# Performance work log

Measured on AMD Instinct MI355X. Metric: run time of the kernel, lower is better.

## Reference

```python
import jax, jax.numpy as jnp
import numpy as np

EPS = 1e-05
HEAD_DIM = 32


def setup_inputs() -> dict:
    key = jax.random.key(0)
    ks = jax.random.split(key, 8)
    b, c, h, w = 8, 512, 64, 64
    s = 1.0 / np.sqrt(c).astype(np.float32)
    return {
        "q": jax.random.normal(ks[0], (b, c, h, w), jnp.float32),
        "k": jax.random.normal(ks[1], (b, c, h, w), jnp.float32),
        "v": jax.random.normal(ks[2], (b, c, h, w), jnp.float32),
        "Wq": jax.random.normal(ks[3], (c, c), jnp.float32) * s,
        "Wk": jax.random.normal(ks[4], (c, c), jnp.float32) * s,
        "Wv": jax.random.normal(ks[5], (c, c), jnp.float32) * s,
        "Wp": jax.random.normal(ks[6], (c, c), jnp.float32) * s,
        "bp": jax.random.normal(ks[7], (c,), jnp.float32) * 0.02,
    }


def reference(q, k, v, Wq, Wk, Wv, Wp, bp):
    b, c, h, w = q.shape
    n = h * w
    hd = HEAD_DIM
    nh = c // hd

    def proj_heads(x, W):
        # NCHW -> (b, n, c) tokens, then Linear (x @ W.T), then split heads
        t = x.reshape(b, c, n).transpose(0, 2, 1)          # (b, n, c)
        y = jnp.einsum('bnc,dc->bnd', t, W)                # torch Linear: x @ W.T
        return y.reshape(b, n, nh, hd)                     # (b, n, h, d)

    # elu feature map: elu(x) + 1
    Q = jax.nn.elu(proj_heads(q, Wq)) + 1.0
    K = jax.nn.elu(proj_heads(k, Wk)) + 1.0
    V = proj_heads(v, Wv)

    # NOTE: faithful to original einsums — KV contracts over HEADS per token,
    # Z uses K summed over the sequence.
    KV = jnp.einsum('bnhd,bnhm->bnmd', K, V)               # (b, n, d_out=m? -> (b,n,hd,hd))
    Z = 1.0 / (jnp.einsum('bnhd,bhd->bnh', Q, K.sum(axis=1)) + EPS)  # (b, n, h)
    out = jnp.einsum('bnhd,bnmd,bnh->bnhm', Q, KV, Z)      # (b, n, h, m)

    out = out.reshape(b, n, c)                             # merge heads
    out = jnp.einsum('bnc,dc->bnd', out, Wp) + bp          # output projection
    return out.transpose(0, 2, 1).reshape(b, c, h, w)
```

## Files before the change

kernel.cpp:

```cpp
#include <hip/hip_runtime.h>
#include <hip/hip_bf16.h>

#define BATCH 8
#define CD 512
#define NT 4096
#define EPSV 1e-5f

using u16x8 = __attribute__((ext_vector_type(8))) unsigned short;
using u16x4 = __attribute__((ext_vector_type(4))) unsigned short;
using bf8   = __attribute__((ext_vector_type(8))) short;
using f32x4 = __attribute__((ext_vector_type(4))) float;

__device__ __forceinline__ float b2f(unsigned short u) {
    union { unsigned int i; float f; } x; x.i = ((unsigned int)u) << 16; return x.f;
}
__device__ __forceinline__ unsigned short f2b(float f) {
    unsigned int x = __float_as_uint(f);
    unsigned int r = (x + 0x7fffu + ((x >> 16) & 1u)) >> 16;
    return (unsigned short)r;
}
__device__ __forceinline__ unsigned int cvtpk(float a, float b) {
    unsigned int r;
    asm("v_cvt_pk_bf16_f32 %0, %1, %2" : "=v"(r) : "v"(a), "v"(b));
    return r;
}
__device__ __forceinline__ void gload_lds16(const void* g, void* l) {
    __builtin_amdgcn_global_load_lds((const __attribute__((address_space(1))) unsigned int*)g,
                                     (__attribute__((address_space(3))) unsigned int*)l, 16, 0, 0);
}
__device__ __forceinline__ int swz8(int r) { return (r ^ (r >> 3)) & 7; }

__global__ __launch_bounds__(256)
void wconv(const float* __restrict__ W0, const float* __restrict__ W1,
           const float* __restrict__ W2, const float* __restrict__ W3,
           unsigned short* __restrict__ Wb) {
    const float* src = (blockIdx.y == 0) ? W0 : (blockIdx.y == 1) ? W1 : (blockIdx.y == 2) ? W2 : W3;
    unsigned short* dst = Wb + (size_t)blockIdx.y * CD * CD;
    const int base = blockIdx.x * 4096 + threadIdx.x * 16;
    u16x8 o0, o1;
    #pragma unroll
    for (int i = 0; i < 4; ++i) {
        float4 v = *reinterpret_cast<const float4*>(src + base + i * 4);
        unsigned short* t = (i < 2) ? (unsigned short*)&o0 : (unsigned short*)&o1;
        t[(i & 1) * 4 + 0] = f2b(v.x); t[(i & 1) * 4 + 1] = f2b(v.y);
        t[(i & 1) * 4 + 2] = f2b(v.z); t[(i & 1) * 4 + 3] = f2b(v.w);
    }
    *(u16x8*)(dst + base)     = o0;
    *(u16x8*)(dst + base + 8) = o1;
}

__global__ __launch_bounds__(256)
void proj_gemm_all(const float* __restrict__ q, const float* __restrict__ k,
                   const float* __restrict__ v, const unsigned short* __restrict__ Wb,
                   unsigned short* __restrict__ Qp, unsigned short* __restrict__ Kp,
                   unsigned short* __restrict__ Vp, float* __restrict__ Kpart) {
    __shared__ __align__(16) unsigned short Xs[64 * 512];
    __shared__ __align__(16) unsigned short Ws[128 * 64];
    const int nper = gridDim.x >> 3;
    const int work = (blockIdx.x & 7) * nper + (blockIdx.x >> 3);
    const int mat  = work / 512;
    const int rem  = work - mat * 512;
    const int b    = rem >> 6;
    const int tile = rem & 63;
    const int n0   = tile * 64;
    const float* Xb = (mat == 0 ? q : mat == 1 ? k : v) + (size_t)b * CD * NT;
    const unsigned short* W = Wb + (size_t)mat * CD * CD;
    unsigned short* Tb = (mat == 0 ? Qp : mat == 1 ? Kp : Vp) + (size_t)b * NT * CD;
    const int act = (mat < 2);

    const int tid = threadIdx.x, lane = tid & 63, wv = tid >> 6;

    #pragma unroll 4
    for (int i = 0; i < 8; ++i) {
        const int s  = i * 256 + tid;
        const int c0 = (s >> 4) * 4;
        const int t0 = (s & 15) * 4;
        const float* p = Xb + (size_t)c0 * NT + n0 + t0;
        float4 r0 = *(const float4*)(p);
        float4 r1 = *(const float4*)(p + NT);
        float4 r2 = *(const float4*)(p + 2 * NT);
        float4 r3 = *(const float4*)(p + 3 * NT);
        float a0[4] = {r0.x, r0.y, r0.z, r0.w};
        float a1[4] = {r1.x, r1.y, r1.z, r1.w};
        float a2[4] = {r2.x, r2.y, r2.z, r2.w};
        float a3[4] = {r3.x, r3.y, r3.z, r3.w};
        #pragma unroll
        for (int j = 0; j < 4; ++j) {
            uint2 u;
            u.x = cvtpk(a0[j], a1[j]);
            u.y = cvtpk(a2[j], a3[j]);
            const int row  = t0 + j;
            const int byte = (row * 1024 + c0 * 2) ^ (swz8(row) << 4);
            *(uint2*)((char*)Xs + byte) = u;
        }
    }
    __syncthreads();

    for (int d0i = 0; d0i < 4; ++d0i) {
        f32x4 acc[4][2];
        #pragma unroll
        for (int m = 0; m < 4; ++m)
            #pragma unroll
            for (int j = 0; j < 2; ++j)
                acc[m][j] = (f32x4){0.f, 0.f, 0.f, 0.f};

        for (int kc = 0; kc < 8; ++kc) {
            #pragma unroll
            for (int it = 0; it < 4; ++it) {
                const int idx = it * 256 + tid;
                const int r = idx >> 3, p = idx & 7;
                gload_lds16(W + (size_t)(d0i * 128 + r) * CD + kc * 64 + (p ^ swz8(r)) * 8,
                            (char*)Ws + idx * 16);
            }
            __syncthreads();
            #pragma unroll
            for (int kk = 0; kk < 2; ++kk) {
                const int kp = kk * 4 + (lane >> 4);
                bf8 af[4], bfr[2];
                #pragma unroll
                for (int m = 0; m < 4; ++m) {
                    const int r = m * 16 + (lane & 15);
                    af[m] = *(const bf8*)((const char*)Xs +
                            ((r * 1024 + kc * 128 + kp * 16) ^ (swz8(r) << 4)));
                }
                #pragma unroll
                for (int j = 0; j < 2; ++j) {
                    const int rw = wv * 32 + j * 16 + (lane & 15);
                    bfr[j] = *(const bf8*)((const char*)Ws + rw * 128 + ((kp ^ swz8(rw)) * 16));
                }
                #pragma unroll
                for (int m = 0; m < 4; ++m)
                    #pragma unroll
                    for (int j = 0; j < 2; ++j)
                        acc[m][j] = __builtin_amdgcn_mfma_f32_16x16x32_bf16(af[m], bfr[j], acc[m][j], 0, 0, 0);
            }
            __syncthreads();
        }

        float kacc[2] = {0.f, 0.f};
        #pragma unroll
        for (int m = 0; m < 4; ++m) {
            const int ib = n0 + m * 16 + ((lane >> 4) << 2);
            #pragma unroll
            for (int j = 0; j < 2; ++j) {
                const int jb = d0i * 128 + wv * 32 + j * 16 + (lane & 15);
                f32x4 vv = acc[m][j];
                #pragma unroll
                for (int r = 0; r < 4; ++r) {
                    float val = vv[r];
                    if (act) val = (val > 0.f) ? (val + 1.f) : __expf(val);
                    if (mat == 1) kacc[j] += val;
                    Tb[(size_t)(ib + r) * CD + jb] = f2b(val);
                }
            }
        }
        if (mat == 1) {
            #pragma unroll
            for (int j = 0; j < 2; ++j) {
                float s = kacc[j];
                s += __shfl_xor(s, 16, 64);
                s += __shfl_xor(s, 32, 64);
                if (lane < 16) {
                    const int jb = d0i * 128 + wv * 32 + j * 16 + lane;
                    Kpart[(size_t)(b * 64 + tile) * CD + jb] = s;
                }
            }
        }
    }
}

__global__ __launch_bounds__(512)
void ksum_red2(const float* __restrict__ Kpart, float* __restrict__ Ks) {
    const int b = blockIdx.x, c = threadIdx.x;
    float s = 0.f;
    #pragma unroll 8
    for (int t = 0; t < 64; ++t) s += Kpart[(size_t)(b * 64 + t) * CD + c];
    Ks[b * CD + c] = s;
}

__global__ __launch_bounds__(256)
void gemm_final(const unsigned short* __restrict__ Wp, const unsigned short* __restrict__ Tm,
                float* __restrict__ out, const float* __restrict__ bias) {
    __shared__ __align__(16) unsigned short Asm[128 * 64];
    __shared__ __align__(16) unsigned short Bsm[128 * 64];
    const int nper = gridDim.x >> 3;
    const int work = (blockIdx.x & 7) * nper + (blockIdx.x >> 3);
    const int i0 = (work & 3) * 128;
    const int j0 = ((work >> 2) & 31) * 128;
    const int b  = work >> 7;
    const unsigned short* Bb = Tm + (size_t)b * NT * CD;
    const int tid  = threadIdx.x;
    const int lane = tid & 63;
    const int wv   = tid >> 6;
    const int wi = wv >> 1, wj = wv & 1;

    f32x4 acc[4][4];
    #pragma unroll
    for (int m = 0; m < 4; ++m)
        #pragma unroll
        for (int j = 0; j < 4; ++j)
            acc[m][j] = (f32x4){0.f, 0.f, 0.f, 0.f};

    for (int k0 = 0; k0 < CD; k0 += 64) {
        #pragma unroll
        for (int it = 0; it < 4; ++it) {
            const int idx = it * 256 + tid;
            const int r = idx >> 3, p = idx & 7;
            const int ps = p ^ (r & 7);
            gload_lds16(Wp + (size_t)(i0 + r) * CD + k0 + ps * 8, (char*)Asm + idx * 16);
            gload_lds16(Bb + (size_t)(j0 + r) * CD + k0 + ps * 8, (char*)Bsm + idx * 16);
        }
        __syncthreads();
        #pragma unroll
        for (int kk = 0; kk < 2; ++kk) {
            bf8 af[4], bfr[4];
            #pragma unroll
            for (int m = 0; m < 4; ++m) {
                const int r  = wi * 64 + m * 16 + (lane & 15);
                const int kp = kk * 4 + (lane >> 4);
                af[m] = *(const bf8*)((const char*)Asm + r * 128 + ((kp ^ (r & 7)) * 16));
            }
            #pragma unroll
            for (int j = 0; j < 4; ++j) {
                const int r  = wj * 64 + j * 16 + (lane & 15);
                const int kp = kk * 4 + (lane >> 4);
                bfr[j] = *(const bf8*)((const char*)Bsm + r * 128 + ((kp ^ (r & 7)) * 16));
            }
            #pragma unroll
            for (int m = 0; m < 4; ++m)
                #pragma unroll
                for (int j = 0; j < 4; ++j)
                    acc[m][j] = __builtin_amdgcn_mfma_f32_16x16x32_bf16(af[m], bfr[j], acc[m][j], 0, 0, 0);
        }
        __syncthreads();
    }

    #pragma unroll
    for (int m = 0; m < 4; ++m) {
        const int ib = i0 + wi * 64 + m * 16 + (lane >> 4) * 4;
        #pragma unroll
        for (int j = 0; j < 4; ++j) {
            const int jb = j0 + wj * 64 + j * 16 + (lane & 15);
            f32x4 v = acc[m][j];
            #pragma unroll
            for (int r = 0; r < 4; ++r)
                out[(size_t)b * CD * NT + (size_t)(ib + r) * NT + jb] = v[r] + bias[ib + r];
        }
    }
}

__global__ __launch_bounds__(256)
void middle2(const unsigned short* __restrict__ Q, const unsigned short* __restrict__ K,
             const unsigned short* __restrict__ V, const float* __restrict__ Ksum,
             unsigned short* __restrict__ T) {
    __shared__ __align__(16) unsigned short sV[4][512];
    __shared__ __align__(16) unsigned short sP[4][16][32];
    const int b = blockIdx.y;
    const int tid = threadIdx.x;
    const int w = tid >> 6, lane = tid & 63;
    const int r16 = lane & 15, g = lane >> 4;
    const int n0 = blockIdx.x * 16 + w * 4;
    const unsigned short* Qb = Q + ((size_t)b * NT + n0) * CD;
    const unsigned short* Kb = K + ((size_t)b * NT + n0) * CD;
    const unsigned short* Vb = V + ((size_t)b * NT + n0) * CD;
    unsigned short* Tb = T + ((size_t)b * NT + n0) * CD;
    const int fragoff = r16 * 32 + g * 8;

    {
        const int r = lane >> 2, cq = lane & 3;
        *(u16x4*)&sP[w][r][16 + cq * 4] = (u16x4){0, 0, 0, 0};
    }

    const float* ksp = Ksum + b * CD + fragoff;
    float ks[8];
    {
        float4 a0 = *(const float4*)ksp;
        float4 a1 = *(const float4*)(ksp + 4);
        ks[0] = a0.x; ks[1] = a0.y; ks[2] = a0.z; ks[3] = a0.w;
        ks[4] = a1.x; ks[5] = a1.y; ks[6] = a1.z; ks[7] = a1.w;
    }
    unsigned short* sVw = &sV[w][0];

    for (int t = 0; t < 4; ++t) {
        asm volatile("s_waitcnt lgkmcnt(0)" ::: "memory");
        __builtin_amdgcn_sched_barrier(0);
        gload_lds16(Vb + (size_t)t * CD + lane * 8, (char*)sVw + lane * 16);

        const bf8 qf = *(const bf8*)(Qb + (size_t)t * CD + fragoff);
        const bf8 kf = *(const bf8*)(Kb + (size_t)t * CD + fragoff);

        f32x4 s = {0.f, 0.f, 0.f, 0.f};
        s = __builtin_amdgcn_mfma_f32_16x16x32_bf16(kf, qf, s, 0, 0, 0);

        float part = 0.f;
        #pragma unroll
        for (int e = 0; e < 8; ++e) part += b2f((unsigned short)qf[e]) * ks[e];
        part += __shfl_xor(part, 16, 64);
        part += __shfl_xor(part, 32, 64);
        const float z = 1.f / (part + EPSV);

        u16x4 pw;
        #pragma unroll
        for (int r = 0; r < 4; ++r) pw[r] = f2b(s[r] * z);
        *(u16x4*)&sP[w][r16][g * 4] = pw;

        asm volatile("s_waitcnt vmcnt(0) lgkmcnt(0)" ::: "memory");
        __builtin_amdgcn_sched_barrier(0);

        const bf8 pb = *(const bf8*)&sP[w][r16][g * 8];
        bf8 va0 = {}, va1 = {};
        if (g < 2) {
            #pragma unroll
            for (int e = 0; e < 8; ++e) {
                va0[e] = (short)sVw[(g * 8 + e) * 32 + r16];
                va1[e] = (short)sVw[(g * 8 + e) * 32 + 16 + r16];
            }
        }

        f32x4 o0 = {0.f, 0.f, 0.f, 0.f}, o1 = {0.f, 0.f, 0.f, 0.f};
        o0 = __builtin_amdgcn_mfma_f32_16x16x32_bf16(va0, pb, o0, 0, 0, 0);
        o1 = __builtin_amdgcn_mfma_f32_16x16x32_bf16(va1, pb, o1, 0, 0, 0);

        u16x4 w0, w1;
        #pragma unroll
        for (int r = 0; r < 4; ++r) { w0[r] = f2b(o0[r]); w1[r] = f2b(o1[r]); }
        *(u16x4*)(Tb + (size_t)t * CD + r16 * 32 + g * 4)      = w0;
        *(u16x4*)(Tb + (size_t)t * CD + r16 * 32 + 16 + g * 4) = w1;
    }
}

extern "C" void kernel_launch(void* const* d_in, const int* in_sizes, int n_in,
                              void* d_out, int out_size, void* d_ws, size_t ws_size,
                              hipStream_t stream) {
    const float* q  = (const float*)d_in[0];
    const float* k  = (const float*)d_in[1];
    const float* v  = (const float*)d_in[2];
    const float* Wq = (const float*)d_in[3];
    const float* Wk = (const float*)d_in[4];
    const float* Wv = (const float*)d_in[5];
    const float* Wp = (const float*)d_in[6];
    const float* bp = (const float*)d_in[7];
    float* out = (float*)d_out;

    const size_t slab = (size_t)BATCH * NT * CD;
    unsigned short* Qp = (unsigned short*)d_ws;
    unsigned short* Kp = Qp + slab;
    unsigned short* Vp = Kp + slab;
    unsigned short* Tm = Vp + slab;
    unsigned short* Wb = Tm + slab;
    float* Kpart = (float*)(Wb + 4 * (size_t)CD * CD);
    float* Ks    = Kpart + (size_t)512 * CD;

    wconv<<<dim3(64, 4), 256, 0, stream>>>(Wq, Wk, Wv, Wp, Wb);

    const unsigned short* Wpb = Wb + (size_t)3 * CD * CD;

    proj_gemm_all<<<1536, 256, 0, stream>>>(q, k, v, Wb, Qp, Kp, Vp, Kpart);

    ksum_red2<<<8, 512, 0, stream>>>(Kpart, Ks);

    middle2<<<dim3(256, 8), 256, 0, stream>>>(Qp, Kp, Vp, Ks, Tm);

    gemm_final<<<1024, 256, 0, stream>>>(Wpb, Tm, out, bp);
}
```

Baseline: 193.7 us.

## Retile projection GEMM to 128x128 output tiles with streamed fp32 activations

The projection kernel now gives each block a 128-token by 128-channel output tile and streams both W and the fp32 activations through LDS in 64-wide K chunks using async global-to-LDS loads. Before, a block staged a full 64x512 bf16 activation slab once and looped over four output-channel chunks. Activations are converted to bf16 at fragment-load time from fp32 LDS. The output stores are also vectorised along channels in 4-element packs. The aim is better MFMA-to-load ratio and more parallel blocks, at the cost of rereading the activations four times (once per d0 tile) and doing unswizzled fp32 LDS reads that may conflict.

```diff
diff --git a/kernel.cpp b/kernel.cpp
--- a/kernel.cpp
+++ b/kernel.cpp
@@ -28,7 +28,6 @@
     __builtin_amdgcn_global_load_lds((const __attribute__((address_space(1))) unsigned int*)g,
                                      (__attribute__((address_space(3))) unsigned int*)l, 16, 0, 0);
 }
-__device__ __forceinline__ int swz8(int r) { return (r ^ (r >> 3)) & 7; }
 
 __global__ __launch_bounds__(256)
 void wconv(const float* __restrict__ W0, const float* __restrict__ W1,
@@ -54,118 +53,116 @@
                    const float* __restrict__ v, const unsigned short* __restrict__ Wb,
                    unsigned short* __restrict__ Qp, unsigned short* __restrict__ Kp,
                    unsigned short* __restrict__ Vp, float* __restrict__ Kpart) {
-    __shared__ __align__(16) unsigned short Xs[64 * 512];
-    __shared__ __align__(16) unsigned short Ws[128 * 64];
+    __shared__ __align__(16) float          Xf[64 * 128];
+    __shared__ __align__(16) unsigned short Wsm[128 * 64];
     const int nper = gridDim.x >> 3;
     const int work = (blockIdx.x & 7) * nper + (blockIdx.x >> 3);
-    const int mat  = work / 512;
-    const int rem  = work - mat * 512;
-    const int b    = rem >> 6;
-    const int tile = rem & 63;
-    const int n0   = tile * 64;
+    const int mat  = work / 1024;
+    const int rem  = work - mat * 1024;
+    const int b    = rem >> 7;
+    const int rem2 = rem & 127;
+    const int nt   = rem2 >> 2;
+    const int d0   = (rem2 & 3) * 128;
+    const int n0   = nt * 128;
     const float* Xb = (mat == 0 ? q : mat == 1 ? k : v) + (size_t)b * CD * NT;
     const unsigned short* W = Wb + (size_t)mat * CD * CD;
     unsigned short* Tb = (mat == 0 ? Qp : mat == 1 ? Kp : Vp) + (size_t)b * NT * CD;
     const int act = (mat < 2);
 
     const int tid = threadIdx.x, lane = tid & 63, wv = tid >> 6;
-
-    #pragma unroll 4
-    for (int i = 0; i < 8; ++i) {
-        const int s  = i * 256 + tid;
-        const int c0 = (s >> 4) * 4;
-        const int t0 = (s & 15) * 4;
-        const float* p = Xb + (size_t)c0 * NT + n0 + t0;
-        float4 r0 = *(const float4*)(p);
-        float4 r1 = *(const float4*)(p + NT);
-        float4 r2 = *(const float4*)(p + 2 * NT);
-        float4 r3 = *(const float4*)(p + 3 * NT);
-        float a0[4] = {r0.x, r0.y, r0.z, r0.w};
-        float a1[4] = {r1.x, r1.y, r1.z, r1.w};
-        float a2[4] = {r2.x, r2.y, r2.z, r2.w};
-        float a3[4] = {r3.x, r3.y, r3.z, r3.w};
+    const int r16 = lane & 15, g = lane >> 4;
+    const int wi = wv >> 1, wj = wv & 1;
+
+    f32x4 acc[4][4];
+    #pragma unroll
+    for (int m = 0; m < 4; ++m)
+        #pragma unroll
+        for (int j = 0; j < 4; ++j)
+            acc[m][j] = (f32x4){0.f, 0.f, 0.f, 0.f};
+
+    for (int k0 = 0; k0 < CD; k0 += 64) {
+        #pragma unroll
+        for (int it = 0; it < 4; ++it) {
+            const int idx = it * 256 + tid;
+            const int r = idx >> 3, p = idx & 7;
+            const int ps = p ^ (r & 7);
+            gload_lds16(W + (size_t)(d0 + r) * CD + k0 + ps * 8, (char*)Wsm + idx * 16);
+        }
+        #pragma unroll
+        for (int it = 0; it < 8; ++it) {
+            const int idx = it * 256 + tid;
+            const int r = idx >> 5, p = idx & 31;
+            gload_lds16(Xb + (size_t)(k0 + r) * NT + n0 + p * 4, (char*)Xf + idx * 16);
+        }
+        __syncthreads();
+        #pragma unroll
+        for (int kk = 0; kk < 2; ++kk) {
+            const int kp = kk * 4 + g;
+            bf8 af[4], bfr[4];
+            #pragma unroll
+            for (int m = 0; m < 4; ++m) {
+                const int r = wi * 64 + m * 16 + r16;
+                af[m] = *(const bf8*)((const char*)Wsm + r * 128 + ((kp ^ (r & 7)) * 16));
+            }
+            #pragma unroll
+            for (int j = 0; j < 4; ++j) {
+                const int n = wj * 64 + j * 16 + r16;
+                const float* xp = Xf + (kk * 32 + g * 8) * 128 + n;
+                union { uint4 u; bf8 h; } cvt;
+                cvt.u.x = cvtpk(xp[0],   xp[128]);
+                cvt.u.y = cvtpk(xp[256], xp[384]);
+                cvt.u.z = cvtpk(xp[512], xp[640]);
+                cvt.u.w = cvtpk(xp[768], xp[896]);
+                bfr[j] = cvt.h;
+            }
+            #pragma unroll
+            for (int m = 0; m < 4; ++m)
+                #pragma unroll
+                for (int j = 0; j < 4; ++j)
+                    acc[m][j] = __builtin_amdgcn_mfma_f32_16x16x32_bf16(af[m], bfr[j], acc[m][j], 0, 0, 0);
+        }
+        __syncthreads();
+    }
+
+    float kacc[4][4];
+    #pragma unroll
+    for (int m = 0; m < 4; ++m)
+        #pragma unroll
+        for (int r = 0; r < 4; ++r)
+            kacc[m][r] = 0.f;
+
+    #pragma unroll
+    for (int m = 0; m < 4; ++m) {
+        const int db = d0 + wi * 64 + m * 16 + g * 4;
         #pragma unroll
         for (int j = 0; j < 4; ++j) {
-            uint2 u;
-            u.x = cvtpk(a0[j], a1[j]);
-            u.y = cvtpk(a2[j], a3[j]);
-            const int row  = t0 + j;
-            const int byte = (row * 1024 + c0 * 2) ^ (swz8(row) << 4);
-            *(uint2*)((char*)Xs + byte) = u;
-        }
-    }
-    __syncthreads();
-
-    for (int d0i = 0; d0i < 4; ++d0i) {
-        f32x4 acc[4][2];
+            const int n = n0 + wj * 64 + j * 16 + r16;
+            f32x4 vv = acc[m][j];
+            u16x4 pk;
+            #pragma unroll
+            for (int r = 0; r < 4; ++r) {
+                float val = vv[r];
+                if (act) val = (val > 0.f) ? (val + 1.f) : __expf(val);
+                if (mat == 1) kacc[m][r] += val;
+                pk[r] = f2b(val);
+            }
+            *(u16x4*)(Tb + (size_t)n * CD + db) = pk;
+        }
+    }
+    if (mat == 1) {
         #pragma unroll
         for (int m = 0; m < 4; ++m)
             #pragma unroll
-            for (int j = 0; j < 2; ++j)
-                acc[m][j] = (f32x4){0.f, 0.f, 0.f, 0.f};
-
-        for (int kc = 0; kc < 8; ++kc) {
-            #pragma unroll
-            for (int it = 0; it < 4; ++it) {
-                const int idx = it * 256 + tid;
-                const int r = idx >> 3, p = idx & 7;
-                gload_lds16(W + (size_t)(d0i * 128 + r) * CD + kc * 64 + (p ^ swz8(r)) * 8,
-                            (char*)Ws + idx * 16);
-            }
-            __syncthreads();
-            #pragma unroll
-            for (int kk = 0; kk < 2; ++kk) {
-                const int kp = kk * 4 + (lane >> 4);
-                bf8 af[4], bfr[2];
-                #pragma unroll
-                for (int m = 0; m < 4; ++m) {
-                    const int r = m * 16 + (lane & 15);
-                    af[m] = *(const bf8*)((const char*)Xs +
-                            ((r * 1024 + kc * 128 + kp * 16) ^ (swz8(r) << 4)));
+            for (int r = 0; r < 4; ++r) {
+                float s = kacc[m][r];
+                s += __shfl_xor(s, 1, 64);
+                s += __shfl_xor(s, 2, 64);
+                s += __shfl_xor(s, 4, 64);
+                s += __shfl_xor(s, 8, 64);
+                if (r16 == 0) {
+                    Kpart[(size_t)(b * 64 + nt * 2 + wj) * CD + d0 + wi * 64 + m * 16 + g * 4 + r] = s;
                 }
-                #pragma unroll
-                for (int j = 0; j < 2; ++j) {
-                    const int rw = wv * 32 + j * 16 + (lane & 15);
-                    bfr[j] = *(const bf8*)((const char*)Ws + rw * 128 + ((kp ^ swz8(rw)) * 16));
-                }
-                #pragma unroll
-                for (int m = 0; m < 4; ++m)
-                    #pragma unroll
-                    for (int j = 0; j < 2; ++j)
-                        acc[m][j] = __builtin_amdgcn_mfma_f32_16x16x32_bf16(af[m], bfr[j], acc[m][j], 0, 0, 0);
-            }
-            __syncthreads();
-        }
-
-        float kacc[2] = {0.f, 0.f};
-        #pragma unroll
-        for (int m = 0; m < 4; ++m) {
-            const int ib = n0 + m * 16 + ((lane >> 4) << 2);
-            #pragma unroll
-            for (int j = 0; j < 2; ++j) {
-                const int jb = d0i * 128 + wv * 32 + j * 16 + (lane & 15);
-                f32x4 vv = acc[m][j];
-                #pragma unroll
-                for (int r = 0; r < 4; ++r) {
-                    float val = vv[r];
-                    if (act) val = (val > 0.f) ? (val + 1.f) : __expf(val);
-                    if (mat == 1) kacc[j] += val;
-                    Tb[(size_t)(ib + r) * CD + jb] = f2b(val);
-                }
-            }
-        }
-        if (mat == 1) {
-            #pragma unroll
-            for (int j = 0; j < 2; ++j) {
-                float s = kacc[j];
-                s += __shfl_xor(s, 16, 64);
-                s += __shfl_xor(s, 32, 64);
-                if (lane < 16) {
-                    const int jb = d0i * 128 + wv * 32 + j * 16 + lane;
-                    Kpart[(size_t)(b * 64 + tile) * CD + jb] = s;
-                }
-            }
-        }
+            }
     }
 }
 
@@ -355,7 +352,7 @@
 
     const unsigned short* Wpb = Wb + (size_t)3 * CD * CD;
 
-    proj_gemm_all<<<1536, 256, 0, stream>>>(q, k, v, Wb, Qp, Kp, Vp, Kpart);
+    proj_gemm_all<<<3072, 256, 0, stream>>>(q, k, v, Wb, Qp, Kp, Vp, Kpart);
 
     ksum_red2<<<8, 512, 0, stream>>>(Kpart, Ks);
 
```

Result: slower. 219.4 us (+13.3%).

## Retile projection GEMM to 256-token by 64-output blocks with K-chunked X staging

Applied to the files above, without the earlier changes.

Each projection block now computes a 256-token by 64-output tile, streaming both X and W through LDS in 64-wide K chunks instead of holding the whole 64x512 X tile resident. This cuts LDS use per block to raise occupancy and lets loads overlap across more resident blocks. In exchange, the fp32 input activations are re-read and re-converted once per output tile (8 times). The grid doubles and the K-sum partials are written per wave.

```diff
diff --git a/kernel.cpp b/kernel.cpp
--- a/kernel.cpp
+++ b/kernel.cpp
@@ -54,116 +54,114 @@
                    const float* __restrict__ v, const unsigned short* __restrict__ Wb,
                    unsigned short* __restrict__ Qp, unsigned short* __restrict__ Kp,
                    unsigned short* __restrict__ Vp, float* __restrict__ Kpart) {
-    __shared__ __align__(16) unsigned short Xs[64 * 512];
-    __shared__ __align__(16) unsigned short Ws[128 * 64];
+    __shared__ __align__(16) unsigned short Xs[256 * 64];
+    __shared__ __align__(16) unsigned short Ws[64 * 64];
     const int nper = gridDim.x >> 3;
     const int work = (blockIdx.x & 7) * nper + (blockIdx.x >> 3);
-    const int mat  = work / 512;
-    const int rem  = work - mat * 512;
-    const int b    = rem >> 6;
-    const int tile = rem & 63;
-    const int n0   = tile * 64;
+    const int mat  = work / 1024;
+    const int rem  = work - mat * 1024;
+    const int b    = rem >> 7;
+    const int rem2 = rem & 127;
+    const int nt   = rem2 >> 3;
+    const int dt   = rem2 & 7;
+    const int n0   = nt * 256;
+    const int d0   = dt * 64;
     const float* Xb = (mat == 0 ? q : mat == 1 ? k : v) + (size_t)b * CD * NT;
     const unsigned short* W = Wb + (size_t)mat * CD * CD;
     unsigned short* Tb = (mat == 0 ? Qp : mat == 1 ? Kp : Vp) + (size_t)b * NT * CD;
     const int act = (mat < 2);
 
     const int tid = threadIdx.x, lane = tid & 63, wv = tid >> 6;
-
-    #pragma unroll 4
-    for (int i = 0; i < 8; ++i) {
-        const int s  = i * 256 + tid;
-        const int c0 = (s >> 4) * 4;
-        const int t0 = (s & 15) * 4;
-        const float* p = Xb + (size_t)c0 * NT + n0 + t0;
-        float4 r0 = *(const float4*)(p);
-        float4 r1 = *(const float4*)(p + NT);
-        float4 r2 = *(const float4*)(p + 2 * NT);
-        float4 r3 = *(const float4*)(p + 3 * NT);
-        float a0[4] = {r0.x, r0.y, r0.z, r0.w};
-        float a1[4] = {r1.x, r1.y, r1.z, r1.w};
-        float a2[4] = {r2.x, r2.y, r2.z, r2.w};
-        float a3[4] = {r3.x, r3.y, r3.z, r3.w};
+    const int r16 = lane & 15, g = lane >> 4;
+
+    f32x4 acc[4][4];
+    #pragma unroll
+    for (int m = 0; m < 4; ++m)
+        #pragma unroll
+        for (int j = 0; j < 4; ++j)
+            acc[m][j] = (f32x4){0.f, 0.f, 0.f, 0.f};
+
+    for (int kc = 0; kc < 8; ++kc) {
+        #pragma unroll
+        for (int it = 0; it < 2; ++it) {
+            const int idx = it * 256 + tid;
+            const int r = idx >> 3, p = idx & 7;
+            gload_lds16(W + (size_t)(d0 + r) * CD + kc * 64 + (p ^ swz8(r)) * 8,
+                        (char*)Ws + idx * 16);
+        }
+        #pragma unroll
+        for (int i = 0; i < 4; ++i) {
+            const int s  = i * 256 + tid;
+            const int cq = s >> 6;
+            const int nq = s & 63;
+            const float* p = Xb + (size_t)(kc * 64 + cq * 4) * NT + n0 + nq * 4;
+            float4 r0 = *(const float4*)(p);
+            float4 r1 = *(const float4*)(p + NT);
+            float4 r2 = *(const float4*)(p + 2 * NT);
+            float4 r3 = *(const float4*)(p + 3 * NT);
+            float a0[4] = {r0.x, r0.y, r0.z, r0.w};
+            float a1[4] = {r1.x, r1.y, r1.z, r1.w};
+            float a2[4] = {r2.x, r2.y, r2.z, r2.w};
+            float a3[4] = {r3.x, r3.y, r3.z, r3.w};
+            #pragma unroll
+            for (int j = 0; j < 4; ++j) {
+                uint2 u;
+                u.x = cvtpk(a0[j], a1[j]);
+                u.y = cvtpk(a2[j], a3[j]);
+                const int row  = nq * 4 + j;
+                const int byte = (row * 128 + cq * 8) ^ (swz8(row) << 4);
+                *(uint2*)((char*)Xs + byte) = u;
+            }
+        }
+        __syncthreads();
+        #pragma unroll
+        for (int kk = 0; kk < 2; ++kk) {
+            const int kp = kk * 4 + g;
+            bf8 af[4], bfr[4];
+            #pragma unroll
+            for (int m = 0; m < 4; ++m) {
+                const int r = wv * 64 + m * 16 + r16;
+                af[m] = *(const bf8*)((const char*)Xs + ((r * 128 + kp * 16) ^ (swz8(r) << 4)));
+            }
+            #pragma unroll
+            for (int j = 0; j < 4; ++j) {
+                const int rw = j * 16 + r16;
+                bfr[j] = *(const bf8*)((const char*)Ws + rw * 128 + ((kp ^ swz8(rw)) * 16));
+            }
+            #pragma unroll
+            for (int m = 0; m < 4; ++m)
+                #pragma unroll
+                for (int j = 0; j < 4; ++j)
+                    acc[m][j] = __builtin_amdgcn_mfma_f32_16x16x32_bf16(af[m], bfr[j], acc[m][j], 0, 0, 0);
+        }
+        __syncthreads();
+    }
+
+    float kacc[4] = {0.f, 0.f, 0.f, 0.f};
+    #pragma unroll
+    for (int m = 0; m < 4; ++m) {
+        const int ib = n0 + wv * 64 + m * 16 + g * 4;
         #pragma unroll
         for (int j = 0; j < 4; ++j) {
-            uint2 u;
-            u.x = cvtpk(a0[j], a1[j]);
-            u.y = cvtpk(a2[j], a3[j]);
-            const int row  = t0 + j;
-            const int byte = (row * 1024 + c0 * 2) ^ (swz8(row) << 4);
-            *(uint2*)((char*)Xs + byte) = u;
-        }
-    }
-    __syncthreads();
-
-    for (int d0i = 0; d0i < 4; ++d0i) {
-        f32x4 acc[4][2];
-        #pragma unroll
-        for (int m = 0; m < 4; ++m)
-            #pragma unroll
-            for (int j = 0; j < 2; ++j)
-                acc[m][j] = (f32x4){0.f, 0.f, 0.f, 0.f};
-
-        for (int kc = 0; kc < 8; ++kc) {
-            #pragma unroll
-            for (int it = 0; it < 4; ++it) {
-                const int idx = it * 256 + tid;
-                const int r = idx >> 3, p = idx & 7;
-                gload_lds16(W + (size_t)(d0i * 128 + r) * CD + kc * 64 + (p ^ swz8(r)) * 8,
-                            (char*)Ws + idx * 16);
-            }
-            __syncthreads();
-            #pragma unroll
-            for (int kk = 0; kk < 2; ++kk) {
-                const int kp = kk * 4 + (lane >> 4);
-                bf8 af[4], bfr[2];
-                #pragma unroll
-                for (int m = 0; m < 4; ++m) {
-                    const int r = m * 16 + (lane & 15);
-                    af[m] = *(const bf8*)((const char*)Xs +
-                            ((r * 1024 + kc * 128 + kp * 16) ^ (swz8(r) << 4)));
-                }
-                #pragma unroll
-                for (int j = 0; j < 2; ++j) {
-                    const int rw = wv * 32 + j * 16 + (lane & 15);
-                    bfr[j] = *(const bf8*)((const char*)Ws + rw * 128 + ((kp ^ swz8(rw)) * 16));
-                }
-                #pragma unroll
-                for (int m = 0; m < 4; ++m)
-                    #pragma unroll
-                    for (int j = 0; j < 2; ++j)
-                        acc[m][j] = __builtin_amdgcn_mfma_f32_16x16x32_bf16(af[m], bfr[j], acc[m][j], 0, 0, 0);
-            }
-            __syncthreads();
-        }
-
-        float kacc[2] = {0.f, 0.f};
-        #pragma unroll
-        for (int m = 0; m < 4; ++m) {
-            const int ib = n0 + m * 16 + ((lane >> 4) << 2);
-            #pragma unroll
-            for (int j = 0; j < 2; ++j) {
-                const int jb = d0i * 128 + wv * 32 + j * 16 + (lane & 15);
-                f32x4 vv = acc[m][j];
-                #pragma unroll
-                for (int r = 0; r < 4; ++r) {
-                    float val = vv[r];
-                    if (act) val = (val > 0.f) ? (val + 1.f) : __expf(val);
-                    if (mat == 1) kacc[j] += val;
-                    Tb[(size_t)(ib + r) * CD + jb] = f2b(val);
-                }
-            }
-        }
-        if (mat == 1) {
-            #pragma unroll
-            for (int j = 0; j < 2; ++j) {
-                float s = kacc[j];
-                s += __shfl_xor(s, 16, 64);
-                s += __shfl_xor(s, 32, 64);
-                if (lane < 16) {
-                    const int jb = d0i * 128 + wv * 32 + j * 16 + lane;
-                    Kpart[(size_t)(b * 64 + tile) * CD + jb] = s;
-                }
+            const int jb = d0 + j * 16 + r16;
+            f32x4 vv = acc[m][j];
+            #pragma unroll
+            for (int r = 0; r < 4; ++r) {
+                float val = vv[r];
+                if (act) val = (val > 0.f) ? (val + 1.f) : __expf(val);
+                if (mat == 1) kacc[j] += val;
+                Tb[(size_t)(ib + r) * CD + jb] = f2b(val);
+            }
+        }
+    }
+    if (mat == 1) {
+        #pragma unroll
+        for (int j = 0; j < 4; ++j) {
+            float s = kacc[j];
+            s += __shfl_xor(s, 16, 64);
+            s += __shfl_xor(s, 32, 64);
+            if (lane < 16) {
+                Kpart[(size_t)(b * 64 + nt * 4 + wv) * CD + d0 + j * 16 + lane] = s;
             }
         }
     }
@@ -355,7 +353,7 @@
 
     const unsigned short* Wpb = Wb + (size_t)3 * CD * CD;
 
-    proj_gemm_all<<<1536, 256, 0, stream>>>(q, k, v, Wb, Qp, Kp, Vp, Kpart);
+    proj_gemm_all<<<3072, 256, 0, stream>>>(q, k, v, Wb, Qp, Kp, Vp, Kpart);
 
     ksum_red2<<<8, 512, 0, stream>>>(Kpart, Ks);
 
```

After: 229.7 us. +18.6%, slower.
